# Performance work log

Hardware: AMD Instinct MI355X
Metric: run time of the kernel (lower is better)

Reference implementation:

```python
import jax, jax.numpy as jnp
import numpy as np

DIM = 256; HEADS = 8; B = 8; N = 128; MLP_HID = 4 * DIM


def _ln(x, g, b):
    m = x.mean(-1, keepdims=True)
    v = ((x - m) ** 2).mean(-1, keepdims=True)
    return (x - m) / jnp.sqrt(v + 1e-5) * g + b


def _mlp(x, W1, b1, W2, b2):
    return jax.nn.relu(x @ W1 + b1) @ W2 + b2


def setup_inputs():
    key = jax.random.key(0)
    ks = iter(jax.random.split(key, 48))
    def p(*shape):
        return jax.random.normal(next(ks), shape, jnp.float32) * 0.02
    inp = {
        'x': jax.random.normal(next(ks), (B, N, DIM), jnp.float32),
        'y': jax.random.normal(next(ks), (B, N, N, DIM), jnp.float32),
        'heads': HEADS,
    }
    for nm in ['q', 'k', 'v', 'e', 'oe', 'on']:
        inp['W' + nm] = p(DIM, DIM)
        inp['b' + nm] = p(DIM)
    for nm in ['ln1', 'ln3', 'ln4', 'ln5', 'ln6']:
        inp[nm + '_g'] = jnp.ones((DIM,), jnp.float32)
        inp[nm + '_b'] = jnp.zeros((DIM,), jnp.float32)
    inp['m1_W1'] = p(DIM, MLP_HID); inp['m1_b1'] = p(MLP_HID)
    inp['m1_W2'] = p(MLP_HID, DIM); inp['m1_b2'] = p(DIM)
    inp['m2_W1'] = p(DIM, MLP_HID); inp['m2_b1'] = p(MLP_HID)
    inp['m2_W2'] = p(MLP_HID, DIM); inp['m2_b2'] = p(DIM)
    return inp


def reference(x, y, heads, Wq, bq, Wk, bk, Wv, bv, We, be, Woe, boe, Won, bon,
              ln1_g, ln1_b, ln3_g, ln3_b, ln4_g, ln4_b, ln5_g, ln5_b, ln6_g, ln6_b,
              m1_W1, m1_b1, m1_W2, m1_b2, m2_W1, m2_b1, m2_W2, m2_b2):
    b, n, c = x.shape
    dk = c // heads
    x1 = _ln(x, ln1_g, ln1_b)
    q = (x1 @ Wq + bq).reshape(b, n, heads, dk)
    k = (x1 @ Wk + bk).reshape(b, n, heads, dk)
    v = (x1 @ Wv + bv).reshape(b, n, heads, dk)
    e = (y @ We + be).reshape(b, n, n, heads, dk)
    # elementwise QK (not a dot product), edge-modulated: (b,n,n,h,dk)
    attn = (q[:, :, None] * k[:, None]) / jnp.sqrt(jnp.float32(dk))
    attn = attn * (e + 1.0) * e
    edge = attn.reshape(b, n, n, c) @ Woe + boe
    attn = jax.nn.softmax(attn, axis=2)  # softmax over key/node axis
    node = (attn * v[:, None]).sum(axis=2).reshape(b, n, c)
    node = node @ Won + bon
    x2 = _ln(x1 + node, ln3_g, ln3_b)
    y2 = _ln(edge + y, ln4_g, ln4_b)
    x_out = _ln(x2 + _mlp(x2, m1_W1, m1_b1, m1_W2, m1_b2), ln5_g, ln5_b)
    y_out = _ln(y2 + _mlp(y2, m2_W1, m2_b1, m2_W2, m2_b2), ln6_g, ln6_b)
    return (x_out, y_out)
```

## Files before the change

kernel.cpp:

```cpp
#include <hip/hip_runtime.h>
#include <hip/hip_bf16.h>


#define DIMC 256
#define NSEQ 128
#define NB 8
#define HID 1024
#define EROWS (NB * NSEQ * NSEQ)

typedef __attribute__((ext_vector_type(8)))  short short8;
typedef __attribute__((ext_vector_type(16))) float f32x16;
typedef __attribute__((ext_vector_type(4)))  float f32x4;

__device__ __forceinline__ short f2bf(float f) {
    union { float f; unsigned u; } v; v.f = f;
    unsigned r = (v.u + 0x7FFF + ((v.u >> 16) & 1)) >> 16;
    return (short)r;
}
__device__ __forceinline__ float bf2f(short s) {
    union { unsigned u; float f; } v; v.u = ((unsigned)(unsigned short)s) << 16;
    return v.f;
}

__device__ __forceinline__ float wave_sum(float v) {
    #pragma unroll
    for (int o = 32; o; o >>= 1) v += __shfl_xor(v, o, 64);
    return v;
}

__device__ __forceinline__ float block_reduce_sum(float v, float* sc, int t) {
    #pragma unroll
    for (int o = 32; o > 0; o >>= 1) v += __shfl_down(v, o, 64);
    __syncthreads();
    if ((t & 63) == 0) sc[t >> 6] = v;
    __syncthreads();
    return sc[0] + sc[1] + sc[2] + sc[3];
}

__global__ __launch_bounds__(256, 2) void k_ln_qkv(
    const float* __restrict__ X, const float* __restrict__ g, const float* __restrict__ be,
    const float* __restrict__ Wq, const float* __restrict__ bq,
    const float* __restrict__ Wk, const float* __restrict__ bk,
    const float* __restrict__ Wv, const float* __restrict__ bv,
    float* __restrict__ X1, float* __restrict__ Q, float* __restrict__ K, float* __restrict__ V)
{
    __shared__ float xs[DIMC];
    __shared__ float red[4];
    const int t = threadIdx.x;
    const int row = blockIdx.x;
    float v = X[(size_t)row * DIMC + t];
    float mu = block_reduce_sum(v, red, t) * (1.f / DIMC);
    float d = v - mu;
    float var = block_reduce_sum(d * d, red, t) * (1.f / DIMC);
    float x1v = d * rsqrtf(var + 1e-5f) * g[t] + be[t];
    xs[t] = x1v;
    X1[(size_t)row * DIMC + t] = x1v;
    __syncthreads();
    float aq = bq[t], ak = bk[t], av = bv[t];
    #pragma unroll 4
    for (int k2 = 0; k2 < DIMC; ++k2) {
        float xv = xs[k2];
        aq = fmaf(xv, Wq[k2 * DIMC + t], aq);
        ak = fmaf(xv, Wk[k2 * DIMC + t], ak);
        av = fmaf(xv, Wv[k2 * DIMC + t], av);
    }
    Q[(size_t)row * DIMC + t] = aq;
    K[(size_t)row * DIMC + t] = ak;
    V[(size_t)row * DIMC + t] = av;
}

__global__ __launch_bounds__(256) void k_transpose_bf16(
    const float* __restrict__ src, short* __restrict__ dst, int M, int N)
{
    __shared__ short tile[32][33];
    const int t = threadIdx.x, tx = t & 31, ty = t >> 5;
    const int bx = blockIdx.x, by = blockIdx.y;
    #pragma unroll
    for (int r = ty; r < 32; r += 8)
        tile[r][tx] = f2bf(src[(size_t)(by * 32 + r) * N + bx * 32 + tx]);
    __syncthreads();
    #pragma unroll
    for (int r = ty; r < 32; r += 8)
        dst[(size_t)(bx * 32 + r) * M + by * 32 + tx] = tile[tx][r];
}

__global__ __launch_bounds__(256) void k_prep_wc(
    const float* __restrict__ W1, const float* __restrict__ W2, short* __restrict__ Wc)
{
    const int h = blockIdx.x, t = threadIdx.x;
    short* dst = Wc + (size_t)h * 32768;
    const int hh = t & 63, kq = t >> 6;
    for (int k0 = 0; k0 < 256; k0 += 4) {
        const int k = k0 + kq;
        float v = W1[(size_t)k * HID + h * 64 + hh];
        dst[hh * 256 + (((k >> 3) ^ (hh & 7)) << 3) + (k & 7)] = f2bf(v);
    }
    short* dst2 = dst + 16384;
    for (int kk = 0; kk < 64; ++kk) {
        float v = W2[(size_t)(h * 64 + kk) * DIMC + t];
        dst2[t * 64 + (((kk >> 3) ^ (t & 7)) << 3) + (kk & 7)] = f2bf(v);
    }
}

__global__ __launch_bounds__(256, 2) void k_e_attn_m(
    const float* __restrict__ Y, const short* __restrict__ WeT,
    const float* __restrict__ be,
    const float* __restrict__ Q, const float* __restrict__ Kp,
    short* __restrict__ ATTb)
{
    __shared__ __align__(16) short As[64][256];
    const int t = threadIdx.x, w = t >> 6, lane = t & 63;
    const int l31 = lane & 31, kg = lane >> 5;
    const size_t R0 = (size_t)blockIdx.x * 64;

    for (int r = w * 16; r < w * 16 + 16; ++r) {
        float4 y4 = *(const float4*)&Y[(R0 + r) * DIMC + lane * 4];
        short4 s4;
        s4.x = f2bf(y4.x); s4.y = f2bf(y4.y); s4.z = f2bf(y4.z); s4.w = f2bf(y4.w);
        *(short4*)&As[r][(((lane >> 1) ^ (r & 7)) << 3) + (lane & 1) * 4] = s4;
    }
    __syncthreads();

    const int rh = (w & 1) * 32, cbase = (w >> 1) * 128;
    const int sw = l31 & 7;
    f32x16 acc[4];
    #pragma unroll
    for (int a = 0; a < 4; ++a)
        #pragma unroll
        for (int i = 0; i < 16; ++i) acc[a][i] = 0.f;

    #pragma unroll
    for (int ks = 0; ks < 16; ++ks) {
        const int gk = 2 * ks + kg;
        short8 a = *(const short8*)&As[rh + l31][(gk ^ sw) * 8];
        #pragma unroll
        for (int tt = 0; tt < 4; ++tt) {
            short8 b = *(const short8*)&WeT[(size_t)(cbase + tt * 32 + l31) * DIMC + gk * 8];
            acc[tt] = __builtin_amdgcn_mfma_f32_32x32x16_bf16(a, b, acc[tt], 0, 0, 0);
        }
    }

    const int m0 = (int)(R0);
    const int qrow = m0 >> 7, bidx = m0 >> 14, jb = m0 & 127;
    const float isq = 0.17677669529663687f;
    #pragma unroll
    for (int tt = 0; tt < 4; ++tt) {
        const int n = cbase + tt * 32 + l31;
        const float qv = Q[(size_t)qrow * DIMC + n];
        const float bb = be[n];
        #pragma unroll
        for (int i = 0; i < 16; ++i) {
            const int row = rh + 4 * kg + (i & 3) + 8 * (i >> 2);
            const float kv = Kp[(size_t)((bidx << 7) + jb + row) * DIMC + n];
            const float e = acc[tt][i] + bb;
            const float qk = qv * kv * isq;
            ATTb[(size_t)(m0 + row) * DIMC + n] = f2bf(qk * (e + 1.f) * e);
        }
    }
}

__global__ __launch_bounds__(256, 2) void k_edge_m(
    const short* __restrict__ ATTb, const short* __restrict__ WoeT,
    const float* __restrict__ boe, float* __restrict__ EDGE)
{
    __shared__ __align__(16) short As[64][256];
    const int t = threadIdx.x, w = t >> 6, lane = t & 63;
    const int l31 = lane & 31, kg = lane >> 5;
    const size_t R0 = (size_t)blockIdx.x * 64;

    #pragma unroll
    for (int it = 0; it < 8; ++it) {
        const int r = w * 16 + it * 2 + kg;
        short8 v = *(const short8*)&ATTb[(R0 + r) * DIMC + l31 * 8];
        *(short8*)&As[r][((l31 ^ (r & 7))) * 8] = v;
    }
    __syncthreads();

    const int rh = (w & 1) * 32, cbase = (w >> 1) * 128;
    const int sw = l31 & 7;
    f32x16 acc[4];
    #pragma unroll
    for (int a = 0; a < 4; ++a)
        #pragma unroll
        for (int i = 0; i < 16; ++i) acc[a][i] = 0.f;

    #pragma unroll
    for (int ks = 0; ks < 16; ++ks) {
        const int gk = 2 * ks + kg;
        short8 a = *(const short8*)&As[rh + l31][(gk ^ sw) * 8];
        #pragma unroll
        for (int tt = 0; tt < 4; ++tt) {
            short8 b = *(const short8*)&WoeT[(size_t)(cbase + tt * 32 + l31) * DIMC + gk * 8];
            acc[tt] = __builtin_amdgcn_mfma_f32_32x32x16_bf16(a, b, acc[tt], 0, 0, 0);
        }
    }

    const int m0 = (int)(R0);
    #pragma unroll
    for (int tt = 0; tt < 4; ++tt) {
        const int n = cbase + tt * 32 + l31;
        const float bb = boe[n];
        #pragma unroll
        for (int i = 0; i < 16; ++i) {
            const int row = rh + 4 * kg + (i & 3) + 8 * (i >> 2);
            EDGE[(size_t)(m0 + row) * DIMC + n] = acc[tt][i] + bb;
        }
    }
}

__global__ __launch_bounds__(256, 2) void k_node_x(
    const short* __restrict__ ATTb, const float* __restrict__ V,
    const float* __restrict__ X1,
    const float* __restrict__ Won, const float* __restrict__ bon,
    const float* __restrict__ g3, const float* __restrict__ b3,
    const float* __restrict__ W1, const float* __restrict__ b1,
    const float* __restrict__ W2, const float* __restrict__ b2,
    const float* __restrict__ g5, const float* __restrict__ b5,
    float* __restrict__ OUTX)
{
    __shared__ float ns[DIMC];
    __shared__ float x2s[DIMC];
    __shared__ float hs[HID];
    __shared__ float red[4];
    const int t = threadIdx.x;
    const int bi = blockIdx.x;
    const int b = bi >> 7;
    const short* arow = ATTb + (size_t)bi * NSEQ * DIMC + t;
    const float* vbase = V + (size_t)b * NSEQ * DIMC + t;
    float mx = -3.4e38f, l = 0.f, acc = 0.f;
    for (int j = 0; j < NSEQ; ++j) {
        float a = bf2f(arow[(size_t)j * DIMC]);
        float vv = vbase[(size_t)j * DIMC];
        if (a > mx) { float sc = __expf(mx - a); l *= sc; acc *= sc; mx = a; }
        float p = __expf(a - mx);
        l += p;
        acc = fmaf(p, vv, acc);
    }
    ns[t] = acc / l;
    __syncthreads();
    float o = bon[t];
    #pragma unroll 4
    for (int k2 = 0; k2 < DIMC; ++k2) o = fmaf(ns[k2], Won[k2 * DIMC + t], o);
    float resid = X1[(size_t)bi * DIMC + t] + o;
    float mu = block_reduce_sum(resid, red, t) * (1.f / DIMC);
    float d = resid - mu;
    float var = block_reduce_sum(d * d, red, t) * (1.f / DIMC);
    float x2 = d * rsqrtf(var + 1e-5f) * g3[t] + b3[t];
    x2s[t] = x2;
    __syncthreads();
    float4 h = *(const float4*)&b1[t * 4];
    for (int k2 = 0; k2 < DIMC; ++k2) {
        float xv = x2s[k2];
        float4 w = *(const float4*)&W1[(size_t)k2 * HID + t * 4];
        h.x = fmaf(xv, w.x, h.x); h.y = fmaf(xv, w.y, h.y);
        h.z = fmaf(xv, w.z, h.z); h.w = fmaf(xv, w.w, h.w);
    }
    h.x = fmaxf(h.x, 0.f); h.y = fmaxf(h.y, 0.f); h.z = fmaxf(h.z, 0.f); h.w = fmaxf(h.w, 0.f);
    *(float4*)&hs[t * 4] = h;
    __syncthreads();
    float o2 = b2[t];
    #pragma unroll 4
    for (int hh = 0; hh < HID; ++hh) o2 = fmaf(hs[hh], W2[(size_t)hh * DIMC + t], o2);
    float r2 = x2 + o2;
    float mu2 = block_reduce_sum(r2, red, t) * (1.f / DIMC);
    float d2 = r2 - mu2;
    float v2 = block_reduce_sum(d2 * d2, red, t) * (1.f / DIMC);
    OUTX[(size_t)bi * DIMC + t] = d2 * rsqrtf(v2 + 1e-5f) * g5[t] + b5[t];
}

__global__ __launch_bounds__(512, 2) void k_mlp_y4(
    float* __restrict__ EY, const float* __restrict__ Y,
    const float* __restrict__ g4, const float* __restrict__ b4,
    const short* __restrict__ Wc, const float* __restrict__ b1v,
    const float* __restrict__ b2v,
    const float* __restrict__ g6, const float* __restrict__ b6)
{
    __shared__ __align__(16) short Wbuf[2][32768];
    __shared__ __align__(16) short Hscr[8][16][72];
    const int t = threadIdx.x;
    const int w = t >> 6, lane = t & 63;
    const int l15 = lane & 15, l4 = lane >> 4;
    const int r7 = l15 & 7;
    const size_t R0 = (size_t)blockIdx.x * 128;

    {
        const float4 gv = *(const float4*)&g4[lane * 4];
        const float4 bv = *(const float4*)&b4[lane * 4];
        const int gk = lane >> 1;
        for (int rr = 0; rr < 16; ++rr) {
            const int r = w * 16 + rr;
            const float4 e4 = *(const float4*)&EY[(R0 + r) * DIMC + lane * 4];
            const float4 y4 = *(const float4*)&Y[(R0 + r) * DIMC + lane * 4];
            float v0 = e4.x + y4.x, v1 = e4.y + y4.y, v2 = e4.z + y4.z, v3 = e4.w + y4.w;
            float mu = wave_sum(v0 + v1 + v2 + v3) * (1.f / DIMC);
            float d0 = v0 - mu, d1 = v1 - mu, d2 = v2 - mu, d3 = v3 - mu;
            float var = wave_sum(d0 * d0 + d1 * d1 + d2 * d2 + d3 * d3) * (1.f / DIMC);
            float rs = rsqrtf(var + 1e-5f);
            short4 s4;
            s4.x = f2bf(d0 * rs * gv.x + bv.x);
            s4.y = f2bf(d1 * rs * gv.y + bv.y);
            s4.z = f2bf(d2 * rs * gv.z + bv.z);
            s4.w = f2bf(d3 * rs * gv.w + bv.w);
            *(short4*)&Wbuf[0][r * 256 + ((gk ^ (rr & 7)) << 3) + (lane & 1) * 4] = s4;
        }
    }

    short8 af[8];
    {
        const int row = w * 16 + l15;
        #pragma unroll
        for (int kt = 0; kt < 8; ++kt)
            af[kt] = *(const short8*)&Wbuf[0][row * 256 + (((kt * 4 + l4) ^ r7) << 3)];
    }

    {
        #pragma unroll
        for (int p = 0; p < 8; ++p) {
            short8 v = *(const short8*)&Wc[p * 4096 + t * 8];
            *(short8*)&Wbuf[1][p * 4096 + t * 8] = v;
        }
    }
    __syncthreads();

    f32x4 acc[16];
    #pragma unroll
    for (int i = 0; i < 16; ++i)
        #pragma unroll
        for (int j = 0; j < 4; ++j) acc[i][j] = 0.f;

    for (int h = 0; h < 16; ++h) {
        const short* Wlds = Wbuf[1 - (h & 1)];
        short8 pf[8];
        if (h < 15) {
            const short* src = Wc + (size_t)(h + 1) * 32768;
            #pragma unroll
            for (int p = 0; p < 8; ++p) pf[p] = *(const short8*)&src[p * 4096 + t * 8];
        }

        f32x4 c1[4];
        #pragma unroll
        for (int i = 0; i < 4; ++i)
            #pragma unroll
            for (int j = 0; j < 4; ++j) c1[i][j] = 0.f;
        #pragma unroll
        for (int kt = 0; kt < 8; ++kt) {
            const int gsw = ((kt * 4 + l4) ^ r7) << 3;
            #pragma unroll
            for (int tt = 0; tt < 4; ++tt) {
                short8 b = *(const short8*)&Wlds[(tt * 16 + l15) * 256 + gsw];
                c1[tt] = __builtin_amdgcn_mfma_f32_16x16x32_bf16(af[kt], b, c1[tt], 0, 0, 0);
            }
        }
        #pragma unroll
        for (int tt = 0; tt < 4; ++tt) {
            const float bb = b1v[h * 64 + tt * 16 + l15];
            #pragma unroll
            for (int j = 0; j < 4; ++j)
                Hscr[w][l4 * 4 + j][tt * 16 + l15] = f2bf(fmaxf(c1[tt][j] + bb, 0.f));
        }
        #pragma unroll
        for (int kt2 = 0; kt2 < 2; ++kt2) {
            short8 hf = *(const short8*)&Hscr[w][l15][kt2 * 32 + l4 * 8];
            const int gsw2 = ((kt2 * 4 + l4) ^ r7) << 3;
            #pragma unroll
            for (int ct = 0; ct < 16; ++ct) {
                short8 b = *(const short8*)&Wlds[16384 + (ct * 16 + l15) * 64 + gsw2];
                acc[ct] = __builtin_amdgcn_mfma_f32_16x16x32_bf16(hf, b, acc[ct], 0, 0, 0);
            }
        }
        if (h < 15) {
            short* dst = Wbuf[h & 1];
            #pragma unroll
            for (int p = 0; p < 8; ++p) *(short8*)&dst[p * 4096 + t * 8] = pf[p];
        }
        __syncthreads();
    }

    {
        const int row = w * 16 + l15;
        #pragma unroll
        for (int kt = 0; kt < 8; ++kt)
            *(short8*)&Wbuf[0][row * 256 + (((kt * 4 + l4) ^ r7) << 3)] = af[kt];
    }
    #pragma unroll
    for (int ct = 0; ct < 16; ++ct) {
        const int col = ct * 16 + l15;
        const float bb = b2v[col];
        const int gl = col >> 3;
        #pragma unroll
        for (int j = 0; j < 4; ++j) {
            const int rloc = l4 * 4 + j;
            short yv = Wbuf[0][(w * 16 + rloc) * 256 + ((gl ^ (rloc & 7)) << 3) + (col & 7)];
            acc[ct][j] += bb + bf2f(yv);
        }
    }
    float sx = 0.f, sy = 0.f, sz = 0.f, sw2 = 0.f;
    #pragma unroll
    for (int ct = 0; ct < 16; ++ct) {
        sx += acc[ct][0]; sy += acc[ct][1]; sz += acc[ct][2]; sw2 += acc[ct][3];
    }
    #pragma unroll
    for (int m = 1; m < 16; m <<= 1) {
        sx += __shfl_xor(sx, m, 64); sy += __shfl_xor(sy, m, 64);
        sz += __shfl_xor(sz, m, 64); sw2 += __shfl_xor(sw2, m, 64);
    }
    const float mu0 = sx * (1.f / DIMC), mu1 = sy * (1.f / DIMC);
    const float mu2 = sz * (1.f / DIMC), mu3 = sw2 * (1.f / DIMC);
    float vx = 0.f, vy = 0.f, vz = 0.f, vw = 0.f;
    #pragma unroll
    for (int ct = 0; ct < 16; ++ct) {
        float d0 = acc[ct][0] - mu0, d1 = acc[ct][1] - mu1;
        float d2 = acc[ct][2] - mu2, d3 = acc[ct][3] - mu3;
        vx += d0 * d0; vy += d1 * d1; vz += d2 * d2; vw += d3 * d3;
    }
    #pragma unroll
    for (int m = 1; m < 16; m <<= 1) {
        vx += __shfl_xor(vx, m, 64); vy += __shfl_xor(vy, m, 64);
        vz += __shfl_xor(vz, m, 64); vw += __shfl_xor(vw, m, 64);
    }
    const float rs0 = rsqrtf(vx * (1.f / DIMC) + 1e-5f);
    const float rs1 = rsqrtf(vy * (1.f / DIMC) + 1e-5f);
    const float rs2 = rsqrtf(vz * (1.f / DIMC) + 1e-5f);
    const float rs3 = rsqrtf(vw * (1.f / DIMC) + 1e-5f);
    #pragma unroll
    for (int ct = 0; ct < 16; ++ct) {
        const int col = ct * 16 + l15;
        const float gg = g6[col], bo = b6[col];
        #pragma unroll
        for (int j = 0; j < 4; ++j) {
            const float mj = (j == 0) ? mu0 : (j == 1) ? mu1 : (j == 2) ? mu2 : mu3;
            const float rj = (j == 0) ? rs0 : (j == 1) ? rs1 : (j == 2) ? rs2 : rs3;
            const int r = w * 16 + l4 * 4 + j;
            EY[(R0 + r) * DIMC + col] = (acc[ct][j] - mj) * rj * gg + bo;
        }
    }
}

extern "C" void kernel_launch(void* const* d_in, const int* in_sizes, int n_in,
                              void* d_out, int out_size, void* d_ws, size_t ws_size,
                              hipStream_t stream) {
    const float* x    = (const float*)d_in[0];
    const float* y    = (const float*)d_in[1];
    const float* Wq   = (const float*)d_in[3];  const float* bq  = (const float*)d_in[4];
    const float* Wk   = (const float*)d_in[5];  const float* bk  = (const float*)d_in[6];
    const float* Wv   = (const float*)d_in[7];  const float* bv  = (const float*)d_in[8];
    const float* We   = (const float*)d_in[9];  const float* be  = (const float*)d_in[10];
    const float* Woe  = (const float*)d_in[11]; const float* boe = (const float*)d_in[12];
    const float* Won  = (const float*)d_in[13]; const float* bon = (const float*)d_in[14];
    const float* ln1g = (const float*)d_in[15]; const float* ln1b = (const float*)d_in[16];
    const float* ln3g = (const float*)d_in[17]; const float* ln3b = (const float*)d_in[18];
    const float* ln4g = (const float*)d_in[19]; const float* ln4b = (const float*)d_in[20];
    const float* ln5g = (const float*)d_in[21]; const float* ln5b = (const float*)d_in[22];
    const float* ln6g = (const float*)d_in[23]; const float* ln6b = (const float*)d_in[24];
    const float* m1W1 = (const float*)d_in[25]; const float* m1b1 = (const float*)d_in[26];
    const float* m1W2 = (const float*)d_in[27]; const float* m1b2 = (const float*)d_in[28];
    const float* m2W1 = (const float*)d_in[29]; const float* m2b1 = (const float*)d_in[30];
    const float* m2W2 = (const float*)d_in[31]; const float* m2b2 = (const float*)d_in[32];

    float* outx = (float*)d_out;
    float* outy = (float*)d_out + NB * NSEQ * DIMC;

    float* ws  = (float*)d_ws;
    float* X1  = ws;
    float* Q   = ws + 262144;
    float* K   = ws + 524288;
    float* V   = ws + 786432;
    short* wsS = (short*)(ws + 1048576);
    short* WeT  = wsS;
    short* WoeT = wsS + 65536;
    short* Wc   = wsS + 131072;
    short* ATTb = wsS + 655360;

    k_transpose_bf16<<<dim3(8, 8),  256, 0, stream>>>(We,   WeT,  DIMC, DIMC);
    k_transpose_bf16<<<dim3(8, 8),  256, 0, stream>>>(Woe,  WoeT, DIMC, DIMC);
    k_prep_wc<<<16, 256, 0, stream>>>(m2W1, m2W2, Wc);

    k_ln_qkv<<<NB * NSEQ, 256, 0, stream>>>(x, ln1g, ln1b, Wq, bq, Wk, bk, Wv, bv, X1, Q, K, V);
    k_e_attn_m<<<EROWS / 64, 256, 0, stream>>>(y, WeT, be, Q, K, ATTb);
    k_edge_m<<<EROWS / 64, 256, 0, stream>>>(ATTb, WoeT, boe, outy);
    k_node_x<<<NB * NSEQ, 256, 0, stream>>>(ATTb, V, X1, Won, bon, ln3g, ln3b,
                                            m1W1, m1b1, m1W2, m1b2, ln5g, ln5b, outx);
    k_mlp_y4<<<EROWS / 128, 512, 0, stream>>>(outy, y, ln4g, ln4b,
                                              Wc, m2b1, m2b2, ln6g, ln6b);
}
```

Measured before the change: 969.0 us.

## Use 32x32 MFMA with 256-row blocks and direct global-to-LDS weight staging

The edge MLP kernel now handles 256 rows per block (32 per wave) using 32x32x16 bf16 MFMAs instead of 16x16x32. Each staged weight chunk is reused across twice as many rows, which halves weight traffic per row and cuts the LDS B-fragment reads per MFMA. Weight prefetch moves from register-staged copies to global_load_lds so no registers are held across the compute. In exchange the accumulator and A-fragment registers double, which raises register pressure and may reduce occupancy, and there are half as many blocks to fill the GPU.

```diff
diff --git a/kernel.cpp b/kernel.cpp
--- a/kernel.cpp
+++ b/kernel.cpp
@@ -268,7 +268,7 @@
     OUTX[(size_t)bi * DIMC + t] = d2 * rsqrtf(v2 + 1e-5f) * g5[t] + b5[t];
 }
 
-__global__ __launch_bounds__(512, 2) void k_mlp_y4(
+__global__ __launch_bounds__(512, 2) void k_mlp_y5(
     float* __restrict__ EY, const float* __restrict__ Y,
     const float* __restrict__ g4, const float* __restrict__ b4,
     const short* __restrict__ Wc, const float* __restrict__ b1v,
@@ -276,22 +276,23 @@
     const float* __restrict__ g6, const float* __restrict__ b6)
 {
     __shared__ __align__(16) short Wbuf[2][32768];
-    __shared__ __align__(16) short Hscr[8][16][72];
+    __shared__ __align__(16) short Hscr[8][32][64];
     const int t = threadIdx.x;
     const int w = t >> 6, lane = t & 63;
-    const int l15 = lane & 15, l4 = lane >> 4;
-    const int r7 = l15 & 7;
-    const size_t R0 = (size_t)blockIdx.x * 128;
+    const int l31 = lane & 31, kg = lane >> 5;
+    const int r7 = l31 & 7;
+    const size_t R0 = (size_t)blockIdx.x * 256;
+    short* Wb = &Wbuf[0][0];
 
     {
         const float4 gv = *(const float4*)&g4[lane * 4];
         const float4 bv = *(const float4*)&b4[lane * 4];
-        const int gk = lane >> 1;
-        for (int rr = 0; rr < 16; ++rr) {
-            const int r = w * 16 + rr;
-            const float4 e4 = *(const float4*)&EY[(R0 + r) * DIMC + lane * 4];
-            const float4 y4 = *(const float4*)&Y[(R0 + r) * DIMC + lane * 4];
-            float v0 = e4.x + y4.x, v1 = e4.y + y4.y, v2 = e4.z + y4.z, v3 = e4.w + y4.w;
+        const int gw = lane >> 1;
+        for (int rr = 0; rr < 32; ++rr) {
+            const int row = w * 32 + rr;
+            const float4 e4 = *(const float4*)&EY[(R0 + row) * DIMC + lane * 4];
+            const float4 y4v = *(const float4*)&Y[(R0 + row) * DIMC + lane * 4];
+            float v0 = e4.x + y4v.x, v1 = e4.y + y4v.y, v2 = e4.z + y4v.z, v3 = e4.w + y4v.w;
             float mu = wave_sum(v0 + v1 + v2 + v3) * (1.f / DIMC);
             float d0 = v0 - mu, d1 = v1 - mu, d2 = v2 - mu, d3 = v3 - mu;
             float var = wave_sum(d0 * d0 + d1 * d1 + d2 * d2 + d3 * d3) * (1.f / DIMC);
@@ -301,137 +302,129 @@
             s4.y = f2bf(d1 * rs * gv.y + bv.y);
             s4.z = f2bf(d2 * rs * gv.z + bv.z);
             s4.w = f2bf(d3 * rs * gv.w + bv.w);
-            *(short4*)&Wbuf[0][r * 256 + ((gk ^ (rr & 7)) << 3) + (lane & 1) * 4] = s4;
-        }
-    }
-
-    short8 af[8];
+            *(short4*)&Wb[row * 256 + ((gw ^ (rr & 7)) << 3) + (lane & 1) * 4] = s4;
+        }
+    }
+    __syncthreads();
+
+    short8 af[16];
     {
-        const int row = w * 16 + l15;
-        #pragma unroll
-        for (int kt = 0; kt < 8; ++kt)
-            af[kt] = *(const short8*)&Wbuf[0][row * 256 + (((kt * 4 + l4) ^ r7) << 3)];
+        const int row = w * 32 + l31;
+        #pragma unroll
+        for (int s = 0; s < 16; ++s)
+            af[s] = *(const short8*)&Wb[row * 256 + (((2 * s + kg) ^ r7) << 3)];
+    }
+    __syncthreads();
+
+    auto stage = [&](int h, int buf) {
+        const char* src = (const char*)Wc + (size_t)h * 65536 + w * 8192 + lane * 16;
+        char* dstb = (char*)&Wbuf[buf][0] + w * 8192;
+        #pragma unroll
+        for (int p = 0; p < 8; ++p) {
+            __builtin_amdgcn_global_load_lds(
+                (const __attribute__((address_space(1))) unsigned*)(src + p * 1024),
+                (__attribute__((address_space(3))) unsigned*)(dstb + p * 1024),
+                16, 0, 0);
+        }
+    };
+    stage(0, 1);
+    __syncthreads();
+
+    f32x16 acc[8];
+    #pragma unroll
+    for (int a = 0; a < 8; ++a)
+        #pragma unroll
+        for (int i = 0; i < 16; ++i) acc[a][i] = 0.f;
+
+    for (int h = 0; h < 16; ++h) {
+        const short* Wlds = &Wbuf[1 - (h & 1)][0];
+        if (h < 15) stage(h + 1, h & 1);
+        const float bb0 = b1v[h * 64 + l31];
+        const float bb1 = b1v[h * 64 + 32 + l31];
+
+        f32x16 c1[2];
+        #pragma unroll
+        for (int a = 0; a < 2; ++a)
+            #pragma unroll
+            for (int i = 0; i < 16; ++i) c1[a][i] = 0.f;
+        #pragma unroll
+        for (int s = 0; s < 16; ++s) {
+            const int g = ((2 * s + kg) ^ r7) << 3;
+            #pragma unroll
+            for (int tt = 0; tt < 2; ++tt) {
+                short8 b = *(const short8*)&Wlds[(tt * 32 + l31) * 256 + g];
+                c1[tt] = __builtin_amdgcn_mfma_f32_32x32x16_bf16(af[s], b, c1[tt], 0, 0, 0);
+            }
+        }
+        #pragma unroll
+        for (int tt = 0; tt < 2; ++tt) {
+            const int cq = tt * 4 + (l31 >> 3), c7 = l31 & 7;
+            const float bb = tt ? bb1 : bb0;
+            #pragma unroll
+            for (int i = 0; i < 16; ++i) {
+                const int row = 4 * kg + (i & 3) + 8 * (i >> 2);
+                Hscr[w][row][((cq ^ (row & 7)) << 3) + c7] =
+                    f2bf(fmaxf(c1[tt][i] + bb, 0.f));
+            }
+        }
+        #pragma unroll
+        for (int s = 0; s < 4; ++s) {
+            const int g2 = ((2 * s + kg) ^ r7) << 3;
+            short8 hf = *(const short8*)&Hscr[w][l31][g2];
+            #pragma unroll
+            for (int ct = 0; ct < 8; ++ct) {
+                short8 b = *(const short8*)&Wlds[16384 + (ct * 32 + l31) * 64 + g2];
+                acc[ct] = __builtin_amdgcn_mfma_f32_32x32x16_bf16(hf, b, acc[ct], 0, 0, 0);
+            }
+        }
+        __syncthreads();
     }
 
     {
-        #pragma unroll
-        for (int p = 0; p < 8; ++p) {
-            short8 v = *(const short8*)&Wc[p * 4096 + t * 8];
-            *(short8*)&Wbuf[1][p * 4096 + t * 8] = v;
-        }
-    }
-    __syncthreads();
-
-    f32x4 acc[16];
-    #pragma unroll
-    for (int i = 0; i < 16; ++i)
-        #pragma unroll
-        for (int j = 0; j < 4; ++j) acc[i][j] = 0.f;
-
-    for (int h = 0; h < 16; ++h) {
-        const short* Wlds = Wbuf[1 - (h & 1)];
-        short8 pf[8];
-        if (h < 15) {
-            const short* src = Wc + (size_t)(h + 1) * 32768;
-            #pragma unroll
-            for (int p = 0; p < 8; ++p) pf[p] = *(const short8*)&src[p * 4096 + t * 8];
-        }
-
-        f32x4 c1[4];
-        #pragma unroll
-        for (int i = 0; i < 4; ++i)
-            #pragma unroll
-            for (int j = 0; j < 4; ++j) c1[i][j] = 0.f;
-        #pragma unroll
-        for (int kt = 0; kt < 8; ++kt) {
-            const int gsw = ((kt * 4 + l4) ^ r7) << 3;
-            #pragma unroll
-            for (int tt = 0; tt < 4; ++tt) {
-                short8 b = *(const short8*)&Wlds[(tt * 16 + l15) * 256 + gsw];
-                c1[tt] = __builtin_amdgcn_mfma_f32_16x16x32_bf16(af[kt], b, c1[tt], 0, 0, 0);
-            }
-        }
-        #pragma unroll
-        for (int tt = 0; tt < 4; ++tt) {
-            const float bb = b1v[h * 64 + tt * 16 + l15];
-            #pragma unroll
-            for (int j = 0; j < 4; ++j)
-                Hscr[w][l4 * 4 + j][tt * 16 + l15] = f2bf(fmaxf(c1[tt][j] + bb, 0.f));
-        }
-        #pragma unroll
-        for (int kt2 = 0; kt2 < 2; ++kt2) {
-            short8 hf = *(const short8*)&Hscr[w][l15][kt2 * 32 + l4 * 8];
-            const int gsw2 = ((kt2 * 4 + l4) ^ r7) << 3;
-            #pragma unroll
-            for (int ct = 0; ct < 16; ++ct) {
-                short8 b = *(const short8*)&Wlds[16384 + (ct * 16 + l15) * 64 + gsw2];
-                acc[ct] = __builtin_amdgcn_mfma_f32_16x16x32_bf16(hf, b, acc[ct], 0, 0, 0);
-            }
-        }
-        if (h < 15) {
-            short* dst = Wbuf[h & 1];
-            #pragma unroll
-            for (int p = 0; p < 8; ++p) *(short8*)&dst[p * 4096 + t * 8] = pf[p];
-        }
-        __syncthreads();
-    }
-
-    {
-        const int row = w * 16 + l15;
-        #pragma unroll
-        for (int kt = 0; kt < 8; ++kt)
-            *(short8*)&Wbuf[0][row * 256 + (((kt * 4 + l4) ^ r7) << 3)] = af[kt];
-    }
-    #pragma unroll
-    for (int ct = 0; ct < 16; ++ct) {
-        const int col = ct * 16 + l15;
+        const int row = w * 32 + l31;
+        #pragma unroll
+        for (int s = 0; s < 16; ++s)
+            *(short8*)&Wb[row * 256 + (((2 * s + kg) ^ r7) << 3)] = af[s];
+    }
+    #pragma unroll
+    for (int ct = 0; ct < 8; ++ct) {
+        const int col = ct * 32 + l31;
         const float bb = b2v[col];
-        const int gl = col >> 3;
-        #pragma unroll
-        for (int j = 0; j < 4; ++j) {
-            const int rloc = l4 * 4 + j;
-            short yv = Wbuf[0][(w * 16 + rloc) * 256 + ((gl ^ (rloc & 7)) << 3) + (col & 7)];
-            acc[ct][j] += bb + bf2f(yv);
-        }
-    }
-    float sx = 0.f, sy = 0.f, sz = 0.f, sw2 = 0.f;
-    #pragma unroll
-    for (int ct = 0; ct < 16; ++ct) {
-        sx += acc[ct][0]; sy += acc[ct][1]; sz += acc[ct][2]; sw2 += acc[ct][3];
-    }
-    #pragma unroll
-    for (int m = 1; m < 16; m <<= 1) {
-        sx += __shfl_xor(sx, m, 64); sy += __shfl_xor(sy, m, 64);
-        sz += __shfl_xor(sz, m, 64); sw2 += __shfl_xor(sw2, m, 64);
-    }
-    const float mu0 = sx * (1.f / DIMC), mu1 = sy * (1.f / DIMC);
-    const float mu2 = sz * (1.f / DIMC), mu3 = sw2 * (1.f / DIMC);
-    float vx = 0.f, vy = 0.f, vz = 0.f, vw = 0.f;
-    #pragma unroll
-    for (int ct = 0; ct < 16; ++ct) {
-        float d0 = acc[ct][0] - mu0, d1 = acc[ct][1] - mu1;
-        float d2 = acc[ct][2] - mu2, d3 = acc[ct][3] - mu3;
-        vx += d0 * d0; vy += d1 * d1; vz += d2 * d2; vw += d3 * d3;
-    }
-    #pragma unroll
-    for (int m = 1; m < 16; m <<= 1) {
-        vx += __shfl_xor(vx, m, 64); vy += __shfl_xor(vy, m, 64);
-        vz += __shfl_xor(vz, m, 64); vw += __shfl_xor(vw, m, 64);
-    }
-    const float rs0 = rsqrtf(vx * (1.f / DIMC) + 1e-5f);
-    const float rs1 = rsqrtf(vy * (1.f / DIMC) + 1e-5f);
-    const float rs2 = rsqrtf(vz * (1.f / DIMC) + 1e-5f);
-    const float rs3 = rsqrtf(vw * (1.f / DIMC) + 1e-5f);
-    #pragma unroll
-    for (int ct = 0; ct < 16; ++ct) {
-        const int col = ct * 16 + l15;
+        const int cq = col >> 3, c7 = col & 7;
+        #pragma unroll
+        for (int i = 0; i < 16; ++i) {
+            const int row = 4 * kg + (i & 3) + 8 * (i >> 2);
+            short yv = Wb[(w * 32 + row) * 256 + ((cq ^ (row & 7)) << 3) + c7];
+            acc[ct][i] += bb + bf2f(yv);
+        }
+    }
+    float mus[16], rss[16];
+    #pragma unroll
+    for (int i = 0; i < 16; ++i) {
+        float s = 0.f;
+        #pragma unroll
+        for (int ct = 0; ct < 8; ++ct) s += acc[ct][i];
+        #pragma unroll
+        for (int m = 1; m < 32; m <<= 1) s += __shfl_xor(s, m, 64);
+        mus[i] = s * (1.f / DIMC);
+    }
+    #pragma unroll
+    for (int i = 0; i < 16; ++i) {
+        float v = 0.f;
+        #pragma unroll
+        for (int ct = 0; ct < 8; ++ct) { float d = acc[ct][i] - mus[i]; v += d * d; }
+        #pragma unroll
+        for (int m = 1; m < 32; m <<= 1) v += __shfl_xor(v, m, 64);
+        rss[i] = rsqrtf(v * (1.f / DIMC) + 1e-5f);
+    }
+    #pragma unroll
+    for (int ct = 0; ct < 8; ++ct) {
+        const int col = ct * 32 + l31;
         const float gg = g6[col], bo = b6[col];
         #pragma unroll
-        for (int j = 0; j < 4; ++j) {
-            const float mj = (j == 0) ? mu0 : (j == 1) ? mu1 : (j == 2) ? mu2 : mu3;
-            const float rj = (j == 0) ? rs0 : (j == 1) ? rs1 : (j == 2) ? rs2 : rs3;
-            const int r = w * 16 + l4 * 4 + j;
-            EY[(R0 + r) * DIMC + col] = (acc[ct][j] - mj) * rj * gg + bo;
+        for (int i = 0; i < 16; ++i) {
+            const int row = 4 * kg + (i & 3) + 8 * (i >> 2);
+            EY[(R0 + w * 32 + row) * DIMC + col] = (acc[ct][i] - mus[i]) * rss[i] * gg + bo;
         }
     }
 }
@@ -480,6 +473,6 @@
     k_edge_m<<<EROWS / 64, 256, 0, stream>>>(ATTb, WoeT, boe, outy);
     k_node_x<<<NB * NSEQ, 256, 0, stream>>>(ATTb, V, X1, Won, bon, ln3g, ln3b,
                                             m1W1, m1b1, m1W2, m1b2, ln5g, ln5b, outx);
-    k_mlp_y4<<<EROWS / 128, 512, 0, stream>>>(outy, y, ln4g, ln4b,
+    k_mlp_y5<<<EROWS / 256, 512, 0, stream>>>(outy, y, ln4g, ln4b,
                                               Wc, m2b1, m2b2, ln6g, ln6b);
 }
```

Measured after the change: 1.004 ms. 1.04x slower.
